# Kernel tuning notes

Hardware: AMD Instinct MI355X
Metric: run time of the kernel (lower is better)

The kernel has to match this reference:

```python
import jax, jax.numpy as jnp
import numpy as np

NEG_SLOPE = 0.01  # F.leaky_relu default in GATLayer.edge_attention
N_NODES = 50000
N_EDGES = 1600000
IN_DIM = 128
HEADS = 8
D_HEAD = 16  # out_dim / head_num = 128 / 8


def setup_inputs() -> dict:
    key = jax.random.key(0)
    ks = jax.random.split(key, 9)
    # glorot-ish scales for linear projections and attention vectors
    w_scale = (2.0 / (IN_DIM + D_HEAD)) ** 0.5
    a_scale = (2.0 / (2 * D_HEAD + 1)) ** 0.5
    return {
        "x": jax.random.normal(ks[0], (N_NODES, IN_DIM), dtype=jnp.float32),
        "src": jax.random.randint(ks[1], (N_EDGES,), 0, N_NODES, dtype=jnp.int32),
        "dst": jax.random.randint(ks[2], (N_EDGES,), 0, N_NODES, dtype=jnp.int32),
        "W1": jax.random.normal(ks[3], (HEADS, IN_DIM, D_HEAD), dtype=jnp.float32) * w_scale,
        "a1_src": jax.random.normal(ks[4], (HEADS, D_HEAD), dtype=jnp.float32) * a_scale,
        "a1_dst": jax.random.normal(ks[5], (HEADS, D_HEAD), dtype=jnp.float32) * a_scale,
        "W2": jax.random.normal(ks[6], (HEADS, IN_DIM, D_HEAD), dtype=jnp.float32) * w_scale,
        "a2_src": jax.random.normal(ks[7], (HEADS, D_HEAD), dtype=jnp.float32) * a_scale,
        "a2_dst": jax.random.normal(ks[8], (HEADS, D_HEAD), dtype=jnp.float32) * a_scale,
    }


def gat_multihead(h, src, dst, W, a_src, a_dst, num_nodes):
    """One MultiHeadLayer(GATLayer) with concat merge. h: [N, Din]."""
    z = jnp.einsum("nd,hdk->nhk", h, W)            # [N,H,Dh] per-head projection
    # attn_fc(cat(z_src, z_dst)) == a_src . z_src + a_dst . z_dst
    s_src = jnp.einsum("nhk,hk->nh", z, a_src)      # [N,H]
    s_dst = jnp.einsum("nhk,hk->nh", z, a_dst)      # [N,H]
    e = jax.nn.leaky_relu(s_src[src] + s_dst[dst], NEG_SLOPE)  # [E,H]
    # segment softmax over incoming edges of each dst node
    e_max = jax.ops.segment_max(e, dst, num_segments=num_nodes)          # [N,H]
    e_max = jnp.where(jnp.isfinite(e_max), e_max, 0.0)                   # empty segments
    w = jnp.exp(e - e_max[dst])                                          # [E,H]
    denom = jax.ops.segment_sum(w, dst, num_segments=num_nodes)          # [N,H]
    msg = w[:, :, None] * z[src]                                         # [E,H,Dh]
    num = jax.ops.segment_sum(msg, dst, num_segments=num_nodes)          # [N,H,Dh]
    out = num / jnp.where(denom == 0.0, 1.0, denom)[:, :, None]
    return out.reshape(num_nodes, -1)                                    # concat heads -> [N, H*Dh]


def reference(x, src, dst, W1, a1_src, a1_dst, W2, a2_src, a2_dst):
    n = x.shape[0]
    h = gat_multihead(x, src, dst, W1, a1_src, a1_dst, n)
    h = jax.nn.elu(h)
    h = gat_multihead(h, src, dst, W2, a2_src, a2_dst, n)
    return h
```

## Files before the change

### kernel.cpp

```cpp
#include <hip/hip_runtime.h>
#include <hip/hip_bf16.h>

#define N_NODES 50000
#define N_EDGES 1600000
#define NEG_SLOPE 0.01f
#define WPAD 136

#define NBKT 256
#define BKTW 196
#define NBLK1 200
#define CHUNK1 8000

typedef _Float16 v8h __attribute__((ext_vector_type(8)));
typedef float v4f __attribute__((ext_vector_type(4)));

__global__ __launch_bounds__(256) void proj_mfma_kernel(
    const float* __restrict__ x,
    const float* __restrict__ W,
    _Float16* __restrict__ z)
{
    __shared__ _Float16 Wl[128 * WPAD];

    const int t = threadIdx.x;
    for (int i = t; i < 16384; i += 256) {
        const int h = i >> 11, k = (i >> 4) & 127, col = i & 15;
        Wl[(h * 16 + col) * WPAD + k] = (_Float16)W[i];
    }
    __syncthreads();

    const int wid = t >> 6;
    const int l   = t & 63;
    const int lc  = l & 15;
    const int kg  = l >> 4;

    const int nwaves = gridDim.x * 4;
    for (int tile = blockIdx.x * 4 + wid; tile < N_NODES / 16; tile += nwaves) {
        const int n0 = tile * 16;
        v4f acc[8];
#pragma unroll
        for (int ht = 0; ht < 8; ht++) acc[ht] = (v4f)0.f;

#pragma unroll
        for (int kb = 0; kb < 4; kb++) {
            const float* xp = &x[(n0 + lc) * 128 + kb * 32 + kg * 8];
            v8h a;
#pragma unroll
            for (int j = 0; j < 8; j++) a[j] = (_Float16)xp[j];
#pragma unroll
            for (int ht = 0; ht < 8; ht++) {
                const v8h b = *(const v8h*)&Wl[(ht * 16 + lc) * WPAD + kb * 32 + kg * 8];
                acc[ht] = __builtin_amdgcn_mfma_f32_16x16x32_f16(a, b, acc[ht], 0, 0, 0);
            }
        }

        _Float16* zp = &z[(n0 + 4 * kg) * 128 + lc];
#pragma unroll
        for (int ht = 0; ht < 8; ht++)
#pragma unroll
            for (int i = 0; i < 4; i++)
                zp[i * 128 + ht * 16] = (_Float16)acc[ht][i];
    }
}

__global__ __launch_bounds__(256) void score_kernel(
    const _Float16* __restrict__ z,
    const float* __restrict__ a_src, const float* __restrict__ a_dst,
    float* __restrict__ s_src, float* __restrict__ s_dst)
{
    __shared__ float asl[128], adl[128];
    const int t = threadIdx.x;
    if (t < 128) { asl[t] = a_src[t]; adl[t] = a_dst[t]; }
    __syncthreads();

    const int idx = blockIdx.x * 256 + t;
    if (idx >= N_NODES * 8) return;
    const int n = idx >> 3, h = idx & 7;

    const v8h z0 = *(const v8h*)&z[n * 128 + h * 16];
    const v8h z1 = *(const v8h*)&z[n * 128 + h * 16 + 8];
    float ss = 0.f, sd = 0.f;
#pragma unroll
    for (int j = 0; j < 8; j++) {
        ss = fmaf((float)z0[j], asl[h * 16 + j], ss);
        sd = fmaf((float)z0[j], adl[h * 16 + j], sd);
    }
#pragma unroll
    for (int j = 0; j < 8; j++) {
        ss = fmaf((float)z1[j], asl[h * 16 + 8 + j], ss);
        sd = fmaf((float)z1[j], adl[h * 16 + 8 + j], sd);
    }
    s_src[idx] = ss;
    s_dst[idx] = sd;
}

__global__ __launch_bounds__(256) void hist_bucket_kernel(
    const int* __restrict__ dst, int* __restrict__ bh)
{
    __shared__ int lhist[NBKT];
    const int t = threadIdx.x, blk = blockIdx.x;
    lhist[t] = 0;
    __syncthreads();
    const int e0 = blk * CHUNK1, e1 = e0 + CHUNK1;
    for (int e = e0 + t; e < e1; e += 256)
        atomicAdd(&lhist[(unsigned)dst[e] / BKTW], 1);
    __syncthreads();
    bh[t * NBLK1 + blk] = lhist[t];
}

__global__ __launch_bounds__(256) void scan_buckets_kernel(
    int* __restrict__ bh, int* __restrict__ btotal)
{
    __shared__ int sb[256];
    const int t = threadIdx.x, b = blockIdx.x;
    const int v = (t < NBLK1) ? bh[b * NBLK1 + t] : 0;
    sb[t] = v;
    __syncthreads();
    int x = v;
    for (int off = 1; off < 256; off <<= 1) {
        const int add = (t >= off) ? sb[t - off] : 0;
        __syncthreads();
        x += add;
        sb[t] = x;
        __syncthreads();
    }
    if (t < NBLK1) bh[b * NBLK1 + t] = x - v;
    if (t == 255) btotal[b] = x;
}

__global__ __launch_bounds__(256) void scan_totals_kernel(
    const int* __restrict__ btotal, int* __restrict__ bstart)
{
    __shared__ int sb[256];
    const int t = threadIdx.x;
    const int v = btotal[t];
    sb[t] = v;
    __syncthreads();
    int x = v;
    for (int off = 1; off < 256; off <<= 1) {
        const int add = (t >= off) ? sb[t - off] : 0;
        __syncthreads();
        x += add;
        sb[t] = x;
        __syncthreads();
    }
    bstart[t] = x - v;
    if (t == 255) bstart[256] = x;
}

__global__ __launch_bounds__(256) void scatter_bucket_kernel(
    const int* __restrict__ src, const int* __restrict__ dst,
    const int* __restrict__ bh, const int* __restrict__ bstart,
    int* __restrict__ gbuf)
{
    __shared__ int lbase[NBKT];
    __shared__ int lcur[NBKT];
    const int t = threadIdx.x, blk = blockIdx.x;
    lbase[t] = bstart[t] + bh[t * NBLK1 + blk];
    lcur[t] = 0;
    __syncthreads();
    const int e0 = blk * CHUNK1, e1 = e0 + CHUNK1;
    for (int e = e0 + t; e < e1; e += 256) {
        const int d = dst[e];
        const unsigned b = (unsigned)d / BKTW;
        const int ld = d - (int)b * BKTW;
        const int r = atomicAdd(&lcur[b], 1);
        gbuf[lbase[b] + r] = (ld << 16) | src[e];
    }
}

__global__ __launch_bounds__(256) void sort_bucket_kernel(
    const int* __restrict__ gbuf, const int* __restrict__ bstart,
    int* __restrict__ perm, int* __restrict__ rowp)
{
    __shared__ int lhist[NBKT];
    __shared__ int lscan[NBKT];
    __shared__ int lcur[NBKT];
    const int t = threadIdx.x, b = blockIdx.x;
    const int base = bstart[b];
    const int cnt  = bstart[b + 1] - base;
    const int n0   = b * BKTW;

    lhist[t] = 0;
    lcur[t] = 0;
    __syncthreads();
    for (int i = t; i < cnt; i += 256)
        atomicAdd(&lhist[gbuf[base + i] >> 16], 1);
    __syncthreads();

    const int v = lhist[t];
    lscan[t] = v;
    __syncthreads();
    int x = v;
    for (int off = 1; off < 256; off <<= 1) {
        const int add = (t >= off) ? lscan[t - off] : 0;
        __syncthreads();
        x += add;
        lscan[t] = x;
        __syncthreads();
    }
    const int excl = x - v;
    __syncthreads();
    lscan[t] = excl;

    const int n = n0 + t;
    if (t < BKTW && n < N_NODES) rowp[n] = base + excl;
    if (b == NBKT - 1 && t == 0) rowp[N_NODES] = bstart[NBKT];
    __syncthreads();

    for (int i = t; i < cnt; i += 256) {
        const int e = gbuf[base + i];
        const int ld = e >> 16;
        const int r = atomicAdd(&lcur[ld], 1);
        perm[base + lscan[ld] + r] = e & 0xFFFF;
    }
}

__global__ __launch_bounds__(128) void gather_kernel(
    const int* __restrict__ row_ptr, const int* __restrict__ perm,
    const _Float16* __restrict__ z,
    const float* __restrict__ s_src, const float* __restrict__ s_dst,
    float* __restrict__ out, const int apply_elu)
{
    __shared__ int   se_l[32];
    __shared__ float w_l[32][9];
    __shared__ float sdl[8];

    const int n = blockIdx.x;
    const int t = threadIdx.x;
    const int c = t;
    const int h = t >> 4;
    const int start = row_ptr[n];
    const int end   = row_ptr[n + 1];
    if (t < 8) sdl[t] = s_dst[n * 8 + t];
    __syncthreads();

    float acc = 0.f, wsum = 0.f;

    for (int j0 = start; j0 < end; j0 += 32) {
        const int cnt = min(32, end - j0);
        __syncthreads();
        {
            const int j = t & 31, hp = t >> 5;
            if (j < cnt) {
                const int se = perm[j0 + j];
                if (hp == 0) se_l[j] = se;
                const float2 sv = *(const float2*)&s_src[se * 8 + hp * 2];
                float s0 = sv.x + sdl[hp * 2];
                float s1 = sv.y + sdl[hp * 2 + 1];
                s0 = s0 > 0.f ? s0 : NEG_SLOPE * s0;
                s1 = s1 > 0.f ? s1 : NEG_SLOPE * s1;
                w_l[j][hp * 2]     = __expf(s0);
                w_l[j][hp * 2 + 1] = __expf(s1);
            }
        }
        __syncthreads();
#pragma unroll 4
        for (int j = 0; j < cnt; j++) {
            const float w = w_l[j][h];
            wsum += w;
            acc = fmaf(w, (float)z[se_l[j] * 128 + c], acc);
        }
    }

    float o = (end > start) ? acc / wsum : 0.f;
    if (apply_elu) o = o > 0.f ? o : expm1f(o);
    out[n * 128 + c] = o;
}

extern "C" void kernel_launch(void* const* d_in, const int* in_sizes, int n_in,
                              void* d_out, int out_size, void* d_ws, size_t ws_size,
                              hipStream_t stream) {
    const float* x    = (const float*)d_in[0];
    const int*   src  = (const int*)d_in[1];
    const int*   dst  = (const int*)d_in[2];
    const float* W1   = (const float*)d_in[3];
    const float* a1s  = (const float*)d_in[4];
    const float* a1d  = (const float*)d_in[5];
    const float* W2   = (const float*)d_in[6];
    const float* a2s  = (const float*)d_in[7];
    const float* a2d  = (const float*)d_in[8];
    float* out = (float*)d_out;

    char* p = (char*)d_ws;
    _Float16* z  = (_Float16*)p;  p += (size_t)N_NODES * 128 * 2;
    float* ssrc  = (float*)p;     p += (size_t)N_NODES * 8 * 4;
    float* sdst  = (float*)p;     p += (size_t)N_NODES * 8 * 4;
    int*   rowp  = (int*)p;       p += ((size_t)N_NODES + 4) * 4;
    int*   bh    = (int*)p;       p += (size_t)NBKT * NBLK1 * 4;
    int*   btot  = (int*)p;       p += (size_t)NBKT * 4;
    int*   bstart= (int*)p;       p += ((size_t)NBKT + 4) * 4;
    int*   gbuf  = (int*)p;       p += (size_t)N_EDGES * 4;
    int*   perm  = (int*)p;       p += (size_t)N_EDGES * 4;

    const int PROJ_GRID  = 391;
    const int SCORE_GRID = (N_NODES * 8 + 255) / 256;

    hist_bucket_kernel<<<NBLK1, 256, 0, stream>>>(dst, bh);
    scan_buckets_kernel<<<NBKT, 256, 0, stream>>>(bh, btot);
    scan_totals_kernel<<<1, 256, 0, stream>>>(btot, bstart);
    scatter_bucket_kernel<<<NBLK1, 256, 0, stream>>>(src, dst, bh, bstart, gbuf);
    sort_bucket_kernel<<<NBKT, 256, 0, stream>>>(gbuf, bstart, perm, rowp);

    proj_mfma_kernel<<<PROJ_GRID, 256, 0, stream>>>(x, W1, z);
    score_kernel<<<SCORE_GRID, 256, 0, stream>>>(z, a1s, a1d, ssrc, sdst);
    gather_kernel<<<N_NODES, 128, 0, stream>>>(rowp, perm, z, ssrc, sdst, out, 1);

    proj_mfma_kernel<<<PROJ_GRID, 256, 0, stream>>>(out, W2, z);
    score_kernel<<<SCORE_GRID, 256, 0, stream>>>(z, a2s, a2d, ssrc, sdst);
    gather_kernel<<<N_NODES, 128, 0, stream>>>(rowp, perm, z, ssrc, sdst, out, 0);
}
```

Before: 251.9 us.

## Restructure gather to one wave per node with prefetched edge chunks

The gather kernel now handles two nodes per 128-thread block, one 64-lane wave per node. This removes the block-wide __syncthreads and relies on in-wave ordering of LDS accesses. Attention weights and source indices for the next 8-edge chunk are computed in registers while the current chunk is accumulated. Each lane handles two channels through packed half2 loads and writes a float2. The projection kernel also loads x rows with float4 reads instead of scalar loads. The risk is extra padded iterations for short segments and a correctness dependence on wave-synchronous LDS behaviour.

```diff
diff --git a/kernel.cpp b/kernel.cpp
--- a/kernel.cpp
+++ b/kernel.cpp
@@ -12,6 +12,7 @@
 #define CHUNK1 8000
 
 typedef _Float16 v8h __attribute__((ext_vector_type(8)));
+typedef _Float16 v2h __attribute__((ext_vector_type(2)));
 typedef float v4f __attribute__((ext_vector_type(4)));
 
 __global__ __launch_bounds__(256) void proj_mfma_kernel(
@@ -42,10 +43,14 @@
 
 #pragma unroll
         for (int kb = 0; kb < 4; kb++) {
-            const float* xp = &x[(n0 + lc) * 128 + kb * 32 + kg * 8];
+            const float4* xp = (const float4*)&x[(n0 + lc) * 128 + kb * 32 + kg * 8];
+            const float4 xa = xp[0];
+            const float4 xb = xp[1];
             v8h a;
-#pragma unroll
-            for (int j = 0; j < 8; j++) a[j] = (_Float16)xp[j];
+            a[0] = (_Float16)xa.x; a[1] = (_Float16)xa.y;
+            a[2] = (_Float16)xa.z; a[3] = (_Float16)xa.w;
+            a[4] = (_Float16)xb.x; a[5] = (_Float16)xb.y;
+            a[6] = (_Float16)xb.z; a[7] = (_Float16)xb.w;
 #pragma unroll
             for (int ht = 0; ht < 8; ht++) {
                 const v8h b = *(const v8h*)&Wl[(ht * 16 + lc) * WPAD + kb * 32 + kg * 8];
@@ -221,50 +226,75 @@
     const float* __restrict__ s_src, const float* __restrict__ s_dst,
     float* __restrict__ out, const int apply_elu)
 {
-    __shared__ int   se_l[32];
-    __shared__ float w_l[32][9];
-    __shared__ float sdl[8];
-
-    const int n = blockIdx.x;
-    const int t = threadIdx.x;
-    const int c = t;
-    const int h = t >> 4;
+    __shared__ int   se_l[2][8];
+    __shared__ float w_l[2][8][8];
+
+    const int t  = threadIdx.x;
+    const int wv = t >> 6;
+    const int l  = t & 63;
+    const int n  = blockIdx.x * 2 + wv;
+
+    const int h8 = l & 7;
+    const int je = l >> 3;
+    const int c0 = 2 * l;
+    const int h  = l >> 3;
+
     const int start = row_ptr[n];
     const int end   = row_ptr[n + 1];
-    if (t < 8) sdl[t] = s_dst[n * 8 + t];
-    __syncthreads();
-
-    float acc = 0.f, wsum = 0.f;
-
-    for (int j0 = start; j0 < end; j0 += 32) {
-        const int cnt = min(32, end - j0);
-        __syncthreads();
+    const float sd  = s_dst[n * 8 + h8];
+
+    float acc0 = 0.f, acc1 = 0.f, wsum = 0.f;
+
+    int   se_r = 0;
+    float w_r  = 0.f;
+    {
+        const int j = start + je;
+        if (j < end) {
+            se_r = perm[j];
+            float s = s_src[se_r * 8 + h8] + sd;
+            s = s > 0.f ? s : NEG_SLOPE * s;
+            w_r = __expf(s);
+        }
+    }
+
+    for (int j0 = start; j0 < end; j0 += 8) {
+        if (h8 == 0) se_l[wv][je] = se_r;
+        w_l[wv][je][h8] = w_r;
+
+        int   se_n = 0;
+        float w_n  = 0.f;
         {
-            const int j = t & 31, hp = t >> 5;
-            if (j < cnt) {
-                const int se = perm[j0 + j];
-                if (hp == 0) se_l[j] = se;
-                const float2 sv = *(const float2*)&s_src[se * 8 + hp * 2];
-                float s0 = sv.x + sdl[hp * 2];
-                float s1 = sv.y + sdl[hp * 2 + 1];
-                s0 = s0 > 0.f ? s0 : NEG_SLOPE * s0;
-                s1 = s1 > 0.f ? s1 : NEG_SLOPE * s1;
-                w_l[j][hp * 2]     = __expf(s0);
-                w_l[j][hp * 2 + 1] = __expf(s1);
+            const int j = j0 + 8 + je;
+            if (j < end) {
+                se_n = perm[j];
+                float s = s_src[se_n * 8 + h8] + sd;
+                s = s > 0.f ? s : NEG_SLOPE * s;
+                w_n = __expf(s);
             }
         }
-        __syncthreads();
-#pragma unroll 4
-        for (int j = 0; j < cnt; j++) {
-            const float w = w_l[j][h];
+
+#pragma unroll
+        for (int j = 0; j < 8; j++) {
+            const float w  = w_l[wv][j][h];
+            const int   se = se_l[wv][j];
+            const v2h   zv = *(const v2h*)&z[se * 128 + c0];
             wsum += w;
-            acc = fmaf(w, (float)z[se_l[j] * 128 + c], acc);
+            acc0 = fmaf(w, (float)zv[0], acc0);
+            acc1 = fmaf(w, (float)zv[1], acc1);
         }
-    }
-
-    float o = (end > start) ? acc / wsum : 0.f;
-    if (apply_elu) o = o > 0.f ? o : expm1f(o);
-    out[n * 128 + c] = o;
+
+        se_r = se_n;
+        w_r  = w_n;
+    }
+
+    const float inv = (wsum > 0.f) ? 1.f / wsum : 0.f;
+    float o0 = acc0 * inv;
+    float o1 = acc1 * inv;
+    if (apply_elu) {
+        o0 = o0 > 0.f ? o0 : expm1f(o0);
+        o1 = o1 > 0.f ? o1 : expm1f(o1);
+    }
+    *(float2*)&out[n * 128 + c0] = make_float2(o0, o1);
 }
 
 extern "C" void kernel_launch(void* const* d_in, const int* in_sizes, int n_in,
@@ -303,9 +333,9 @@
 
     proj_mfma_kernel<<<PROJ_GRID, 256, 0, stream>>>(x, W1, z);
     score_kernel<<<SCORE_GRID, 256, 0, stream>>>(z, a1s, a1d, ssrc, sdst);
-    gather_kernel<<<N_NODES, 128, 0, stream>>>(rowp, perm, z, ssrc, sdst, out, 1);
+    gather_kernel<<<N_NODES / 2, 128, 0, stream>>>(rowp, perm, z, ssrc, sdst, out, 1);
 
     proj_mfma_kernel<<<PROJ_GRID, 256, 0, stream>>>(out, W2, z);
     score_kernel<<<SCORE_GRID, 256, 0, stream>>>(z, a2s, a2d, ssrc, sdst);
-    gather_kernel<<<N_NODES, 128, 0, stream>>>(rowp, perm, z, ssrc, sdst, out, 0);
-}
+    gather_kernel<<<N_NODES / 2, 128, 0, stream>>>(rowp, perm, z, ssrc, sdst, out, 0);
+}
```

Result: faster. 218.8 us (-13.1%).
